# Optimization experiments

Hardware: AMD Instinct MI355X
Metric: run time of the kernel (lower is better)

## Reference

```python
import jax, jax.numpy as jnp
import numpy as np

N, D, E = 16384, 2048, 64          # tokens, d_model, n_experts
G = 8                               # n_expert_group
TOP_K = 8                           # experts selected per token
TOP_K_GROUP = 4                     # groups selected per token


def setup_inputs() -> dict:
    key = jax.random.key(0)
    k1, k2 = jax.random.split(key)
    x = jax.random.normal(k1, (N, D), dtype=jnp.float32)
    W = jax.random.normal(k2, (E, D), dtype=jnp.float32) * 0.02  # Linear weight
    b = jnp.zeros((E,), dtype=jnp.float32)                        # Linear bias
    bias = jnp.zeros((1, E), dtype=jnp.float32)                   # aux-loss-free routing bias
    return {"x": x, "W": W, "b": b, "bias": bias}


def reference(x, W, b, bias):
    n = x.shape[0]
    # linear + sigmoid
    score2weights = jax.nn.sigmoid(x @ W.T + b)       # [N, E]
    score = score2weights + bias                      # routing score with bias
    # group view
    score_g = score.reshape(n, G, -1)                 # [N, G, E/G]
    w_g = score2weights.reshape(n, G, -1)
    # group score = sum of top min(2, top_k) expert scores within each group
    top2, _ = jax.lax.top_k(score_g, min(2, TOP_K))   # [N, G, 2]
    group_score = top2.sum(axis=-1)                   # [N, G]
    # select top groups, build group mask (scatter)
    _, gidx = jax.lax.top_k(group_score, TOP_K_GROUP) # [N, TOP_K_GROUP]
    mask = jnp.zeros((n, G), score.dtype).at[jnp.arange(n)[:, None], gidx].set(1.0)
    # mask out non-selected groups, flatten back to expert dim
    score_m = (score_g * mask[..., None]).reshape(n, -1)   # [N, E]
    w_m = (w_g * mask[..., None]).reshape(n, -1)
    # final per-token expert selection + weight gather
    _, idx = jax.lax.top_k(score_m, TOP_K)            # [N, TOP_K] int32
    weights = jnp.take_along_axis(w_m, idx, axis=1)   # [N, TOP_K]
    return weights, idx
```

## Files before the change

kernel.cpp:

```cpp
#include <hip/hip_runtime.h>
#include <math.h>

#define DIM   2048
#define NEXP  64
#define NGRP  8
#define GSIZE 8
#define TOPK  8
#define TOPKG 4

#define TPB1  1024
#define NKS   8
#define KSL   (DIM / NKS)
#define SMSTR 1092

#define TAU_E 6e-5f
#define TAU_G 1.2e-4f
#define NEG_INF (-3.4e38f)
#define WLOFF 16
#define WT_OFF (1 << 18)

typedef __attribute__((ext_vector_type(8)))  short bf16x8;
typedef __attribute__((ext_vector_type(16))) float f32x16;

union FragU { bf16x8 v; unsigned short u[8]; };

static __device__ __forceinline__ unsigned short bf16_rne(float f) {
    unsigned u = __builtin_bit_cast(unsigned, f);
    u += 0x7FFFu + ((u >> 16) & 1u);
    return (unsigned short)(u >> 16);
}
static __device__ __forceinline__ float bf16_to_f(unsigned short h) {
    unsigned u = ((unsigned)h) << 16;
    return __builtin_bit_cast(float, u);
}

__global__ __launch_bounds__(256) void prep_kernel(
    const float* __restrict__ W, unsigned short* __restrict__ Wf,
    int* __restrict__ wl)
{
    const int g = blockIdx.x * 256 + threadIdx.x;
    const int e = g >> 11, k = g & 2047;
    const float w = W[g];
    const unsigned short hi = bf16_rne(w);
    const unsigned short lo = bf16_rne(w - bf16_to_f(hi));
    const int n2 = e >> 5, lcol = e & 31;
    const int kc = k >> 4, khalf = (k >> 3) & 1, j = k & 7;
    const int lane = (khalf << 5) | lcol;
    Wf[((((0 * 2 + n2) * 128 + kc) << 6) + lane) * 8 + j] = hi;
    Wf[((((1 * 2 + n2) * 128 + kc) << 6) + lane) * 8 + j] = lo;
    if (g < WLOFF) wl[g] = 0;
}

__global__ __launch_bounds__(TPB1, 4) void gate_kernel(
    const float* __restrict__ x,
    const unsigned short* __restrict__ Wf,
    const float* __restrict__ b,
    const float* __restrict__ bias,
    float* __restrict__ out_w,
    float* __restrict__ out_i,
    int* __restrict__ wl)
{
    __shared__ float sM[NKS * SMSTR];
    __shared__ float sS[64][65];

    const int tid  = threadIdx.x;
    const int w    = tid >> 6;
    const int lane = tid & 63;
    const int m    = w >> 3;
    const int ks   = w & 7;
    const int tok0 = blockIdx.x * 64;
    const int l31  = lane & 31, lh = lane >> 5;

    const float* xr = x + (size_t)(tok0 + 32 * m + l31) * DIM + ks * KSL + lh * 8;
    const bf16x8* Wfv = (const bf16x8*)Wf;

    f32x16 acc0, acc1;
#pragma unroll
    for (int z = 0; z < 16; ++z) { acc0[z] = 0.f; acc1[z] = 0.f; }

    float4 p0 = *(const float4*)(xr + 0);
    float4 p1 = *(const float4*)(xr + 4);
    float4 p2 = *(const float4*)(xr + 16);
    float4 p3 = *(const float4*)(xr + 20);

#pragma unroll 1
    for (int i = 0; i < 8; ++i) {
        const float4 c00 = p0, c01 = p1, c10 = p2, c11 = p3;
        if (i + 1 < 8) {
            p0 = *(const float4*)(xr + 32 * (i + 1) + 0);
            p1 = *(const float4*)(xr + 32 * (i + 1) + 4);
            p2 = *(const float4*)(xr + 32 * (i + 1) + 16);
            p3 = *(const float4*)(xr + 32 * (i + 1) + 20);
        }
        const int kc0 = ks * 16 + 2 * i;

#pragma unroll
        for (int c = 0; c < 2; ++c) {
            const int kc = kc0 + c;
            const float4 qa = c ? c10 : c00;
            const float4 qb = c ? c11 : c01;
            const float xv[8] = {qa.x, qa.y, qa.z, qa.w, qb.x, qb.y, qb.z, qb.w};
            FragU ah, al;
#pragma unroll
            for (int j = 0; j < 8; ++j) {
                const unsigned short h = bf16_rne(xv[j]);
                ah.u[j] = (short)h;
                al.u[j] = (short)bf16_rne(xv[j] - bf16_to_f(h));
            }
            const bf16x8 bh0 = Wfv[((0 * 2 + 0) * 128 + kc) * 64 + lane];
            const bf16x8 bh1 = Wfv[((0 * 2 + 1) * 128 + kc) * 64 + lane];
            const bf16x8 bl0 = Wfv[((1 * 2 + 0) * 128 + kc) * 64 + lane];
            const bf16x8 bl1 = Wfv[((1 * 2 + 1) * 128 + kc) * 64 + lane];

            acc0 = __builtin_amdgcn_mfma_f32_32x32x16_bf16(ah.v, bh0, acc0, 0, 0, 0);
            acc0 = __builtin_amdgcn_mfma_f32_32x32x16_bf16(ah.v, bl0, acc0, 0, 0, 0);
            acc0 = __builtin_amdgcn_mfma_f32_32x32x16_bf16(al.v, bh0, acc0, 0, 0, 0);
            acc1 = __builtin_amdgcn_mfma_f32_32x32x16_bf16(ah.v, bh1, acc1, 0, 0, 0);
            acc1 = __builtin_amdgcn_mfma_f32_32x32x16_bf16(ah.v, bl1, acc1, 0, 0, 0);
            acc1 = __builtin_amdgcn_mfma_f32_32x32x16_bf16(al.v, bh1, acc1, 0, 0, 0);
        }
    }

#pragma unroll
    for (int r = 0; r < 4; ++r) {
#pragma unroll
        for (int jj = 0; jj < 4; ++jj) {
            const int t16 = 8 * m + jj + 4 * lh;
            sM[ks * SMSTR + t16 * 68 + l31]      = acc0[4 * r + jj];
            sM[ks * SMSTR + t16 * 68 + l31 + 32] = acc1[4 * r + jj];
        }
        __syncthreads();
        {
            const int t16 = tid >> 6;
            const int e   = tid & 63;
            float sum = 0.f;
#pragma unroll
            for (int s = 0; s < NKS; ++s)
                sum += sM[s * SMSTR + t16 * 68 + e];
            const float logit = sum + b[e];
            const float wv = 1.0f / (1.0f + expf(-logit));
            const int t_blk = 32 * (t16 >> 3) + 8 * r + (t16 & 7);
            sS[t_blk][e] = wv + bias[e];
        }
        __syncthreads();
    }

    if (tid < 64) {
        const int t = tid;

        float gs[NGRP];
#pragma unroll
        for (int g = 0; g < NGRP; ++g) {
            float m1 = NEG_INF, m2 = NEG_INF;
#pragma unroll
            for (int j = 0; j < GSIZE; ++j) {
                const float v = sS[t][g * GSIZE + j];
                if (v > m1) { m2 = m1; m1 = v; }
                else if (v > m2) { m2 = v; }
            }
            gs[g] = m1 + m2;
        }

        unsigned gmask = 0u;
        float g4val = NEG_INF;
        for (int rr = 0; rr < TOPKG; ++rr) {
            float best = NEG_INF; int bi = 0;
#pragma unroll
            for (int g = 0; g < NGRP; ++g) {
                const float v = ((gmask >> g) & 1u) ? NEG_INF : gs[g];
                if (v > best) { best = v; bi = g; }
            }
            gmask |= 1u << bi;
            g4val = best;
        }
        float m5 = NEG_INF;
#pragma unroll
        for (int g = 0; g < NGRP; ++g)
            if (!((gmask >> g) & 1u) && gs[g] > m5) m5 = gs[g];
        const float margin_g = g4val - m5;

        unsigned long long chosen = 0ull;
        const size_t obase = (size_t)(tok0 + t) * TOPK;
        float vals[TOPK + 1];
        for (int rr = 0; rr < TOPK + 1; ++rr) {
            float best = NEG_INF; int bi = 0;
            for (int e = 0; e < NEXP; ++e) {
                float v = ((gmask >> (e >> 3)) & 1u) ? sS[t][e] : 0.0f;
                if ((chosen >> e) & 1ull) v = NEG_INF;
                if (v > best) { best = v; bi = e; }
            }
            vals[rr] = best;
            if (rr < TOPK) {
                chosen |= 1ull << (unsigned)bi;
                out_w[obase + rr] = ((gmask >> (bi >> 3)) & 1u)
                                  ? (sS[t][bi] - bias[bi]) : 0.0f;
                out_i[obase + rr] = (float)bi;
            }
        }
        float margin_e = 1e30f;
#pragma unroll
        for (int rr = 0; rr < TOPK; ++rr) {
            const float d = vals[rr] - vals[rr + 1];
            if (d < margin_e) margin_e = d;
        }

        if (margin_g < TAU_G || margin_e < TAU_E) {
            const int slot = atomicAdd(wl, 1);
            wl[WLOFF + slot] = tok0 + t;
        }
    }
}

__global__ __launch_bounds__(256) void gate_fix_kernel(
    const float* __restrict__ x,
    const float* __restrict__ W,
    const float* __restrict__ b,
    const float* __restrict__ bias,
    float* __restrict__ out_w,
    float* __restrict__ out_i,
    const int* __restrict__ wl)
{
    const int count = wl[0];

    __shared__ __align__(16) float sX[DIM];
    __shared__ double sPart[NEXP][4];
    __shared__ float  sS2[NEXP], sW2[NEXP];

    const int tid = threadIdx.x;
    const int e   = tid >> 2;
    const int s   = tid & 3;

    for (int widx = blockIdx.x; widx < count; widx += (int)gridDim.x) {
        const int tok = wl[WLOFF + widx];

        const float4* xr = (const float4*)(x + (size_t)tok * DIM);
        ((float4*)sX)[tid]       = xr[tid];
        ((float4*)sX)[tid + 256] = xr[tid + 256];
        __syncthreads();

        const float4* Wr = (const float4*)(W + (size_t)e * DIM);
        double a0 = 0., a1 = 0., a2 = 0., a3 = 0.;
#pragma unroll 8
        for (int mm = 0; mm < DIM / 16; ++mm) {
            const int c = mm * 4 + s;
            const float4 wv = Wr[c];
            const float4 xv = ((const float4*)sX)[c];
            a0 = fma((double)xv.x, (double)wv.x, a0);
            a1 = fma((double)xv.y, (double)wv.y, a1);
            a2 = fma((double)xv.z, (double)wv.z, a2);
            a3 = fma((double)xv.w, (double)wv.w, a3);
        }
        sPart[e][s] = (a0 + a1) + (a2 + a3);
        __syncthreads();

        if (tid < NEXP) {
            const double logit = ((sPart[tid][0] + sPart[tid][1])
                                + (sPart[tid][2] + sPart[tid][3])) + (double)b[tid];
            const float wv = (float)(1.0 / (1.0 + exp(-logit)));
            sW2[tid] = wv;
            sS2[tid] = wv + bias[tid];
        }
        __syncthreads();

        if (tid == 0) {
            float gs[NGRP];
#pragma unroll
            for (int g = 0; g < NGRP; ++g) {
                float m1 = NEG_INF, m2 = NEG_INF;
#pragma unroll
                for (int j = 0; j < GSIZE; ++j) {
                    const float v = sS2[g * GSIZE + j];
                    if (v > m1) { m2 = m1; m1 = v; }
                    else if (v > m2) { m2 = v; }
                }
                gs[g] = m1 + m2;
            }
            unsigned gmask = 0u;
            for (int rr = 0; rr < TOPKG; ++rr) {
                float best = NEG_INF; int bi = 0;
#pragma unroll
                for (int g = 0; g < NGRP; ++g) {
                    const float v = ((gmask >> g) & 1u) ? NEG_INF : gs[g];
                    if (v > best) { best = v; bi = g; }
                }
                gmask |= 1u << bi;
            }
            unsigned long long chosen = 0ull;
            const size_t obase = (size_t)tok * TOPK;
            for (int rr = 0; rr < TOPK; ++rr) {
                float best = NEG_INF; int bi = 0;
                for (int e2 = 0; e2 < NEXP; ++e2) {
                    float v = ((gmask >> (e2 >> 3)) & 1u) ? sS2[e2] : 0.0f;
                    if ((chosen >> e2) & 1ull) v = NEG_INF;
                    if (v > best) { best = v; bi = e2; }
                }
                chosen |= 1ull << (unsigned)bi;
                out_w[obase + rr] = ((gmask >> (bi >> 3)) & 1u) ? sW2[bi] : 0.0f;
                out_i[obase + rr] = (float)bi;
            }
        }
        __syncthreads();
    }
}

extern "C" void kernel_launch(void* const* d_in, const int* in_sizes, int n_in,
                              void* d_out, int out_size, void* d_ws, size_t ws_size,
                              hipStream_t stream) {
    const float* x    = (const float*)d_in[0];
    const float* W    = (const float*)d_in[1];
    const float* b    = (const float*)d_in[2];
    const float* bias = (const float*)d_in[3];

    const int n = in_sizes[0] / DIM;
    float* out_w = (float*)d_out;
    float* out_i = out_w + (size_t)n * TOPK;
    int*   wl    = (int*)d_ws;
    unsigned short* Wf = (unsigned short*)((char*)d_ws + WT_OFF);

    prep_kernel<<<dim3((NEXP * DIM) / 256), dim3(256), 0, stream>>>(W, Wf, wl);
    gate_kernel<<<dim3(n / 64), dim3(TPB1), 0, stream>>>(
        x, Wf, b, bias, out_w, out_i, wl);
    gate_fix_kernel<<<dim3(1024), dim3(256), 0, stream>>>(
        x, W, b, bias, out_w, out_i, wl);
}
```

Baseline: 279.5 us.

## Switch split GEMM to fp16 hi/lo, split routing kernel, per-wave fixup

Replaces the bf16 hi/lo split with fp16 hi/lo (packed RTZ conversion of x), which carries more mantissa bits, so the near-tie thresholds for the exact-recompute fallback are tightened. The fused gate kernel is split into a GEMM kernel (32 tokens per 512-thread block) that writes biased scores to workspace and a separate routing kernel that does the top-k selection. The fallback kernel now handles one token per wave instead of one per block, reading x directly from global memory. Risks include fp16 overflow or underflow on x values and an extra global round trip for the score matrix.

```diff
diff --git a/kernel.cpp b/kernel.cpp
--- a/kernel.cpp
+++ b/kernel.cpp
@@ -8,31 +8,19 @@
 #define TOPK  8
 #define TOPKG 4
 
-#define TPB1  1024
 #define NKS   8
 #define KSL   (DIM / NKS)
-#define SMSTR 1092
-
-#define TAU_E 6e-5f
-#define TAU_G 1.2e-4f
+#define SMSTR 548
+
+#define TAU_E 2e-5f
+#define TAU_G 4e-5f
 #define NEG_INF (-3.4e38f)
 #define WLOFF 16
 #define WT_OFF (1 << 18)
-
-typedef __attribute__((ext_vector_type(8)))  short bf16x8;
-typedef __attribute__((ext_vector_type(16))) float f32x16;
-
-union FragU { bf16x8 v; unsigned short u[8]; };
-
-static __device__ __forceinline__ unsigned short bf16_rne(float f) {
-    unsigned u = __builtin_bit_cast(unsigned, f);
-    u += 0x7FFFu + ((u >> 16) & 1u);
-    return (unsigned short)(u >> 16);
-}
-static __device__ __forceinline__ float bf16_to_f(unsigned short h) {
-    unsigned u = ((unsigned)h) << 16;
-    return __builtin_bit_cast(float, u);
-}
+#define SG_OFF (1 << 20)
+
+typedef __attribute__((ext_vector_type(8)))  _Float16 f16x8;
+typedef __attribute__((ext_vector_type(16))) float    f32x16;
 
 __global__ __launch_bounds__(256) void prep_kernel(
     const float* __restrict__ W, unsigned short* __restrict__ Wf,
@@ -41,38 +29,35 @@
     const int g = blockIdx.x * 256 + threadIdx.x;
     const int e = g >> 11, k = g & 2047;
     const float w = W[g];
-    const unsigned short hi = bf16_rne(w);
-    const unsigned short lo = bf16_rne(w - bf16_to_f(hi));
+    const _Float16 hi = (_Float16)w;
+    const _Float16 lo = (_Float16)(w - (float)hi);
     const int n2 = e >> 5, lcol = e & 31;
     const int kc = k >> 4, khalf = (k >> 3) & 1, j = k & 7;
     const int lane = (khalf << 5) | lcol;
-    Wf[((((0 * 2 + n2) * 128 + kc) << 6) + lane) * 8 + j] = hi;
-    Wf[((((1 * 2 + n2) * 128 + kc) << 6) + lane) * 8 + j] = lo;
+    Wf[((((0 * 2 + n2) * 128 + kc) << 6) + lane) * 8 + j] =
+        __builtin_bit_cast(unsigned short, hi);
+    Wf[((((1 * 2 + n2) * 128 + kc) << 6) + lane) * 8 + j] =
+        __builtin_bit_cast(unsigned short, lo);
     if (g < WLOFF) wl[g] = 0;
 }
 
-__global__ __launch_bounds__(TPB1, 4) void gate_kernel(
+__global__ __launch_bounds__(512, 2) void gemm_kernel(
     const float* __restrict__ x,
     const unsigned short* __restrict__ Wf,
     const float* __restrict__ b,
     const float* __restrict__ bias,
-    float* __restrict__ out_w,
-    float* __restrict__ out_i,
-    int* __restrict__ wl)
+    float* __restrict__ sSg)
 {
     __shared__ float sM[NKS * SMSTR];
-    __shared__ float sS[64][65];
 
     const int tid  = threadIdx.x;
-    const int w    = tid >> 6;
+    const int ks   = tid >> 6;
     const int lane = tid & 63;
-    const int m    = w >> 3;
-    const int ks   = w & 7;
-    const int tok0 = blockIdx.x * 64;
+    const int tok0 = blockIdx.x * 32;
     const int l31  = lane & 31, lh = lane >> 5;
 
-    const float* xr = x + (size_t)(tok0 + 32 * m + l31) * DIM + ks * KSL + lh * 8;
-    const bf16x8* Wfv = (const bf16x8*)Wf;
+    const float* xr = x + (size_t)(tok0 + l31) * DIM + ks * KSL + lh * 8;
+    const f16x8* Wfv = (const f16x8*)Wf;
 
     f32x16 acc0, acc1;
 #pragma unroll
@@ -100,24 +85,26 @@
             const float4 qa = c ? c10 : c00;
             const float4 qb = c ? c11 : c01;
             const float xv[8] = {qa.x, qa.y, qa.z, qa.w, qb.x, qb.y, qb.z, qb.w};
-            FragU ah, al;
-#pragma unroll
-            for (int j = 0; j < 8; ++j) {
-                const unsigned short h = bf16_rne(xv[j]);
-                ah.u[j] = (short)h;
-                al.u[j] = (short)bf16_rne(xv[j] - bf16_to_f(h));
-            }
-            const bf16x8 bh0 = Wfv[((0 * 2 + 0) * 128 + kc) * 64 + lane];
-            const bf16x8 bh1 = Wfv[((0 * 2 + 1) * 128 + kc) * 64 + lane];
-            const bf16x8 bl0 = Wfv[((1 * 2 + 0) * 128 + kc) * 64 + lane];
-            const bf16x8 bl1 = Wfv[((1 * 2 + 1) * 128 + kc) * 64 + lane];
-
-            acc0 = __builtin_amdgcn_mfma_f32_32x32x16_bf16(ah.v, bh0, acc0, 0, 0, 0);
-            acc0 = __builtin_amdgcn_mfma_f32_32x32x16_bf16(ah.v, bl0, acc0, 0, 0, 0);
-            acc0 = __builtin_amdgcn_mfma_f32_32x32x16_bf16(al.v, bh0, acc0, 0, 0, 0);
-            acc1 = __builtin_amdgcn_mfma_f32_32x32x16_bf16(ah.v, bh1, acc1, 0, 0, 0);
-            acc1 = __builtin_amdgcn_mfma_f32_32x32x16_bf16(ah.v, bl1, acc1, 0, 0, 0);
-            acc1 = __builtin_amdgcn_mfma_f32_32x32x16_bf16(al.v, bh1, acc1, 0, 0, 0);
+            f16x8 ah, al;
+#pragma unroll
+            for (int j = 0; j < 8; j += 2) {
+                const auto h2 = __builtin_amdgcn_cvt_pkrtz(xv[j], xv[j + 1]);
+                const auto l2 = __builtin_amdgcn_cvt_pkrtz(xv[j]     - (float)h2.x,
+                                                           xv[j + 1] - (float)h2.y);
+                ah[j] = h2.x; ah[j + 1] = h2.y;
+                al[j] = l2.x; al[j + 1] = l2.y;
+            }
+            const f16x8 bh0 = Wfv[((0 * 2 + 0) * 128 + kc) * 64 + lane];
+            const f16x8 bh1 = Wfv[((0 * 2 + 1) * 128 + kc) * 64 + lane];
+            const f16x8 bl0 = Wfv[((1 * 2 + 0) * 128 + kc) * 64 + lane];
+            const f16x8 bl1 = Wfv[((1 * 2 + 1) * 128 + kc) * 64 + lane];
+
+            acc0 = __builtin_amdgcn_mfma_f32_32x32x16_f16(ah, bh0, acc0, 0, 0, 0);
+            acc0 = __builtin_amdgcn_mfma_f32_32x32x16_f16(ah, bl0, acc0, 0, 0, 0);
+            acc0 = __builtin_amdgcn_mfma_f32_32x32x16_f16(al, bh0, acc0, 0, 0, 0);
+            acc1 = __builtin_amdgcn_mfma_f32_32x32x16_f16(ah, bh1, acc1, 0, 0, 0);
+            acc1 = __builtin_amdgcn_mfma_f32_32x32x16_f16(ah, bl1, acc1, 0, 0, 0);
+            acc1 = __builtin_amdgcn_mfma_f32_32x32x16_f16(al, bh1, acc1, 0, 0, 0);
         }
     }
 
@@ -125,27 +112,52 @@
     for (int r = 0; r < 4; ++r) {
 #pragma unroll
         for (int jj = 0; jj < 4; ++jj) {
-            const int t16 = 8 * m + jj + 4 * lh;
-            sM[ks * SMSTR + t16 * 68 + l31]      = acc0[4 * r + jj];
-            sM[ks * SMSTR + t16 * 68 + l31 + 32] = acc1[4 * r + jj];
+            const int t8 = jj + 4 * lh;
+            sM[ks * SMSTR + t8 * 68 + l31]      = acc0[4 * r + jj];
+            sM[ks * SMSTR + t8 * 68 + l31 + 32] = acc1[4 * r + jj];
         }
         __syncthreads();
         {
-            const int t16 = tid >> 6;
+            const int row = tid >> 6;
             const int e   = tid & 63;
             float sum = 0.f;
 #pragma unroll
             for (int s = 0; s < NKS; ++s)
-                sum += sM[s * SMSTR + t16 * 68 + e];
+                sum += sM[s * SMSTR + row * 68 + e];
             const float logit = sum + b[e];
             const float wv = 1.0f / (1.0f + expf(-logit));
-            const int t_blk = 32 * (t16 >> 3) + 8 * r + (t16 & 7);
-            sS[t_blk][e] = wv + bias[e];
+            sSg[(size_t)(tok0 + 8 * r + row) * NEXP + e] = wv + bias[e];
         }
         __syncthreads();
     }
-
-    if (tid < 64) {
+}
+
+__global__ __launch_bounds__(256) void route_kernel(
+    const float* __restrict__ sSg,
+    const float* __restrict__ bias,
+    float* __restrict__ out_w,
+    float* __restrict__ out_i,
+    int* __restrict__ wl)
+{
+    __shared__ float sT[128][65];
+
+    const int tid  = threadIdx.x;
+    const int tok0 = blockIdx.x * 128;
+
+    const float4* S4 = (const float4*)sSg + (size_t)tok0 * (NEXP / 4);
+#pragma unroll
+    for (int q = 0; q < 8; ++q) {
+        const int idx = q * 256 + tid;
+        const int tk  = idx >> 4, c4 = idx & 15;
+        const float4 v = S4[idx];
+        sT[tk][c4 * 4 + 0] = v.x;
+        sT[tk][c4 * 4 + 1] = v.y;
+        sT[tk][c4 * 4 + 2] = v.z;
+        sT[tk][c4 * 4 + 3] = v.w;
+    }
+    __syncthreads();
+
+    if (tid < 128) {
         const int t = tid;
 
         float gs[NGRP];
@@ -154,7 +166,7 @@
             float m1 = NEG_INF, m2 = NEG_INF;
 #pragma unroll
             for (int j = 0; j < GSIZE; ++j) {
-                const float v = sS[t][g * GSIZE + j];
+                const float v = sT[t][g * GSIZE + j];
                 if (v > m1) { m2 = m1; m1 = v; }
                 else if (v > m2) { m2 = v; }
             }
@@ -185,7 +197,7 @@
         for (int rr = 0; rr < TOPK + 1; ++rr) {
             float best = NEG_INF; int bi = 0;
             for (int e = 0; e < NEXP; ++e) {
-                float v = ((gmask >> (e >> 3)) & 1u) ? sS[t][e] : 0.0f;
+                float v = ((gmask >> (e >> 3)) & 1u) ? sT[t][e] : 0.0f;
                 if ((chosen >> e) & 1ull) v = NEG_INF;
                 if (v > best) { best = v; bi = e; }
             }
@@ -193,7 +205,7 @@
             if (rr < TOPK) {
                 chosen |= 1ull << (unsigned)bi;
                 out_w[obase + rr] = ((gmask >> (bi >> 3)) & 1u)
-                                  ? (sS[t][bi] - bias[bi]) : 0.0f;
+                                  ? (sT[t][bi] - bias[bi]) : 0.0f;
                 out_i[obase + rr] = (float)bi;
             }
         }
@@ -222,84 +234,95 @@
 {
     const int count = wl[0];
 
-    __shared__ __align__(16) float sX[DIM];
-    __shared__ double sPart[NEXP][4];
-    __shared__ float  sS2[NEXP], sW2[NEXP];
-
-    const int tid = threadIdx.x;
-    const int e   = tid >> 2;
-    const int s   = tid & 3;
-
-    for (int widx = blockIdx.x; widx < count; widx += (int)gridDim.x) {
+    __shared__ float sS2[4][NEXP];
+    __shared__ float sW2[4][NEXP];
+
+    const int tid  = threadIdx.x;
+    const int wv_  = tid >> 6;
+    const int lane = tid & 63;
+    const int gw   = blockIdx.x * 4 + wv_;
+
+    const float4* Wr = (const float4*)(W + (size_t)lane * DIM);
+
+    for (int widx = gw; widx < count; widx += (int)gridDim.x * 4) {
         const int tok = wl[WLOFF + widx];
-
         const float4* xr = (const float4*)(x + (size_t)tok * DIM);
-        ((float4*)sX)[tid]       = xr[tid];
-        ((float4*)sX)[tid + 256] = xr[tid + 256];
-        __syncthreads();
-
-        const float4* Wr = (const float4*)(W + (size_t)e * DIM);
+
         double a0 = 0., a1 = 0., a2 = 0., a3 = 0.;
-#pragma unroll 8
-        for (int mm = 0; mm < DIM / 16; ++mm) {
-            const int c = mm * 4 + s;
-            const float4 wv = Wr[c];
-            const float4 xv = ((const float4*)sX)[c];
-            a0 = fma((double)xv.x, (double)wv.x, a0);
-            a1 = fma((double)xv.y, (double)wv.y, a1);
-            a2 = fma((double)xv.z, (double)wv.z, a2);
-            a3 = fma((double)xv.w, (double)wv.w, a3);
-        }
-        sPart[e][s] = (a0 + a1) + (a2 + a3);
-        __syncthreads();
-
-        if (tid < NEXP) {
-            const double logit = ((sPart[tid][0] + sPart[tid][1])
-                                + (sPart[tid][2] + sPart[tid][3])) + (double)b[tid];
-            const float wv = (float)(1.0 / (1.0 + exp(-logit)));
-            sW2[tid] = wv;
-            sS2[tid] = wv + bias[tid];
-        }
-        __syncthreads();
-
-        if (tid == 0) {
-            float gs[NGRP];
+#pragma unroll 4
+        for (int c = 0; c < DIM / 16; ++c) {
+            const float4 x0 = xr[4 * c + 0], w0 = Wr[4 * c + 0];
+            const float4 x1 = xr[4 * c + 1], w1 = Wr[4 * c + 1];
+            const float4 x2 = xr[4 * c + 2], w2 = Wr[4 * c + 2];
+            const float4 x3 = xr[4 * c + 3], w3 = Wr[4 * c + 3];
+            a0 = fma((double)x0.x, (double)w0.x, a0);
+            a0 = fma((double)x0.y, (double)w0.y, a0);
+            a0 = fma((double)x0.z, (double)w0.z, a0);
+            a0 = fma((double)x0.w, (double)w0.w, a0);
+            a1 = fma((double)x1.x, (double)w1.x, a1);
+            a1 = fma((double)x1.y, (double)w1.y, a1);
+            a1 = fma((double)x1.z, (double)w1.z, a1);
+            a1 = fma((double)x1.w, (double)w1.w, a1);
+            a2 = fma((double)x2.x, (double)w2.x, a2);
+            a2 = fma((double)x2.y, (double)w2.y, a2);
+            a2 = fma((double)x2.z, (double)w2.z, a2);
+            a2 = fma((double)x2.w, (double)w2.w, a2);
+            a3 = fma((double)x3.x, (double)w3.x, a3);
+            a3 = fma((double)x3.y, (double)w3.y, a3);
+            a3 = fma((double)x3.z, (double)w3.z, a3);
+            a3 = fma((double)x3.w, (double)w3.w, a3);
+        }
+        const double logit = ((a0 + a1) + (a2 + a3)) + (double)b[lane];
+        const float wvv = (float)(1.0 / (1.0 + exp(-logit)));
+        sW2[wv_][lane] = wvv;
+        sS2[wv_][lane] = wvv + bias[lane];
+        asm volatile("s_waitcnt lgkmcnt(0)" ::: "memory");
+        __builtin_amdgcn_wave_barrier();
+
+        float gsv[NGRP];
+#pragma unroll
+        for (int g = 0; g < NGRP; ++g) {
+            float m1 = NEG_INF, m2 = NEG_INF;
+#pragma unroll
+            for (int j = 0; j < GSIZE; ++j) {
+                const float v = sS2[wv_][g * GSIZE + j];
+                if (v > m1) { m2 = m1; m1 = v; }
+                else if (v > m2) { m2 = v; }
+            }
+            gsv[g] = m1 + m2;
+        }
+        unsigned gmask = 0u;
+        for (int rr = 0; rr < TOPKG; ++rr) {
+            float best = NEG_INF; int bi = 0;
 #pragma unroll
             for (int g = 0; g < NGRP; ++g) {
-                float m1 = NEG_INF, m2 = NEG_INF;
-#pragma unroll
-                for (int j = 0; j < GSIZE; ++j) {
-                    const float v = sS2[g * GSIZE + j];
-                    if (v > m1) { m2 = m1; m1 = v; }
-                    else if (v > m2) { m2 = v; }
-                }
-                gs[g] = m1 + m2;
-            }
-            unsigned gmask = 0u;
-            for (int rr = 0; rr < TOPKG; ++rr) {
-                float best = NEG_INF; int bi = 0;
-#pragma unroll
-                for (int g = 0; g < NGRP; ++g) {
-                    const float v = ((gmask >> g) & 1u) ? NEG_INF : gs[g];
-                    if (v > best) { best = v; bi = g; }
-                }
-                gmask |= 1u << bi;
-            }
-            unsigned long long chosen = 0ull;
+                const float v = ((gmask >> g) & 1u) ? NEG_INF : gsv[g];
+                if (v > best) { best = v; bi = g; }
+            }
+            gmask |= 1u << bi;
+        }
+        unsigned long long chosen = 0ull;
+        float rw[TOPK]; int ri[TOPK];
+        for (int rr = 0; rr < TOPK; ++rr) {
+            float best = NEG_INF; int bi = 0;
+            for (int e2 = 0; e2 < NEXP; ++e2) {
+                float v = ((gmask >> (e2 >> 3)) & 1u) ? sS2[wv_][e2] : 0.0f;
+                if ((chosen >> e2) & 1ull) v = NEG_INF;
+                if (v > best) { best = v; bi = e2; }
+            }
+            chosen |= 1ull << (unsigned)bi;
+            rw[rr] = ((gmask >> (bi >> 3)) & 1u) ? sW2[wv_][bi] : 0.0f;
+            ri[rr] = bi;
+        }
+        if (lane == 0) {
             const size_t obase = (size_t)tok * TOPK;
+#pragma unroll
             for (int rr = 0; rr < TOPK; ++rr) {
-                float best = NEG_INF; int bi = 0;
-                for (int e2 = 0; e2 < NEXP; ++e2) {
-                    float v = ((gmask >> (e2 >> 3)) & 1u) ? sS2[e2] : 0.0f;
-                    if ((chosen >> e2) & 1ull) v = NEG_INF;
-                    if (v > best) { best = v; bi = e2; }
-                }
-                chosen |= 1ull << (unsigned)bi;
-                out_w[obase + rr] = ((gmask >> (bi >> 3)) & 1u) ? sW2[bi] : 0.0f;
-                out_i[obase + rr] = (float)bi;
-            }
-        }
-        __syncthreads();
+                out_w[obase + rr] = rw[rr];
+                out_i[obase + rr] = (float)ri[rr];
+            }
+        }
+        __builtin_amdgcn_wave_barrier();
     }
 }
 
@@ -316,10 +339,12 @@
     float* out_i = out_w + (size_t)n * TOPK;
     int*   wl    = (int*)d_ws;
     unsigned short* Wf = (unsigned short*)((char*)d_ws + WT_OFF);
+    float* sSg   = (float*)((char*)d_ws + SG_OFF);
 
     prep_kernel<<<dim3((NEXP * DIM) / 256), dim3(256), 0, stream>>>(W, Wf, wl);
-    gate_kernel<<<dim3(n / 64), dim3(TPB1), 0, stream>>>(
-        x, Wf, b, bias, out_w, out_i, wl);
-    gate_fix_kernel<<<dim3(1024), dim3(256), 0, stream>>>(
+    gemm_kernel<<<dim3(n / 32), dim3(512), 0, stream>>>(x, Wf, b, bias, sSg);
+    route_kernel<<<dim3(n / 128), dim3(256), 0, stream>>>(
+        sSg, bias, out_w, out_i, wl);
+    gate_fix_kernel<<<dim3(256), dim3(256), 0, stream>>>(
         x, W, b, bias, out_w, out_i, wl);
 }
```

After: 340.8 us. 1.22x slower.
